# Performance work log

Measured on AMD Instinct MI355X. Metric: run time of the kernel, lower is better.

The kernel has to match this reference:

```python
import jax, jax.numpy as jnp
import numpy as np

S, D, H, G, DH = 2048, 4096, 32, 8, 128  # seq, d_in, heads, kv_groups, head_dim
GROUP = H // G


def rotate_half(x):
    x1, x2 = jnp.split(x, 2, axis=-1)
    return jnp.concatenate([-x2, x1], axis=-1)


def setup_inputs() -> dict:
    key = jax.random.key(0)
    ks = jax.random.split(key, 8)
    x = jax.random.normal(ks[0], (1, S, D), dtype=jnp.float32)
    # causal mask: True above the diagonal (positions to mask out)
    mask = jnp.triu(jnp.ones((S, S), dtype=bool), k=1)
    # standard RoPE tables
    inv_freq = 1.0 / (10000.0 ** (np.arange(0, DH, 2, dtype=np.float32) / DH))
    t = np.arange(S, dtype=np.float32)
    freqs = np.outer(t, inv_freq)                      # [S, DH/2]
    emb = np.concatenate([freqs, freqs], axis=-1)      # [S, DH]
    cos = jnp.asarray(np.cos(emb), dtype=jnp.float32)
    sin = jnp.asarray(np.sin(emb), dtype=jnp.float32)
    sc = 0.02
    Wq = jax.random.normal(ks[1], (D, H * DH), dtype=jnp.float32) * sc
    Wk = jax.random.normal(ks[2], (D, G * DH), dtype=jnp.float32) * sc
    Wv = jax.random.normal(ks[3], (D, G * DH), dtype=jnp.float32) * sc
    Wo = jax.random.normal(ks[4], (H * DH, D), dtype=jnp.float32) * sc
    return {"x": x, "mask": mask, "cos": cos, "sin": sin,
            "Wq": Wq, "Wk": Wk, "Wv": Wv, "Wo": Wo}


def reference(x, mask, cos, sin, Wq, Wk, Wv, Wo):
    xs = x[0]                                          # [S, D] (batch must be 1)
    q = (xs @ Wq).reshape(S, H, DH).transpose(1, 0, 2)   # [H, S, DH]
    k = (xs @ Wk).reshape(S, G, DH).transpose(1, 0, 2)   # [G, S, DH]
    v = (xs @ Wv).reshape(S, G, DH).transpose(1, 0, 2)   # [G, S, DH]
    # RoPE
    q = q * cos[None] + rotate_half(q) * sin[None]
    k = k * cos[None] + rotate_half(k) * sin[None]
    # GQA: repeat KV groups to match query heads
    k = jnp.repeat(k, GROUP, axis=0)                   # [H, S, DH]
    v = jnp.repeat(v, GROUP, axis=0)                   # [H, S, DH]
    scores = jnp.einsum('hsd,htd->hst', q, k)          # [H, S, S]
    scores = jnp.where(mask[None], -jnp.inf, scores)
    scores = scores / jnp.sqrt(jnp.float32(DH))
    w = jax.nn.softmax(scores, axis=-1)
    ctx = jnp.einsum('hst,htd->hsd', w, v)             # [H, S, DH]
    ctx = ctx.transpose(1, 0, 2).reshape(S, H * DH)
    out = ctx @ Wo                                     # [S, D]
    return out[None]                                   # [1, S, D]
```

## Files before the change

kernel.cpp:

```cpp
#include <hip/hip_runtime.h>
#include <hip/hip_bf16.h>
#include <cstdint>
#include <cstddef>

#define S 2048
#define D 4096
#define H 32
#define G 8
#define DH 128
#define HD (H*DH)
#define GD (G*DH)

typedef __bf16 bf16;
typedef __bf16 bf16x4 __attribute__((ext_vector_type(4)));
typedef __bf16 bf16x8 __attribute__((ext_vector_type(8)));
typedef float f32x4 __attribute__((ext_vector_type(4)));

__device__ __forceinline__ void gload16(const void* g, void* l) {
    __builtin_amdgcn_global_load_lds(
        (const __attribute__((address_space(1))) void*)g,
        (__attribute__((address_space(3))) void*)l, 16, 0, 0);
}

#define FENCE() asm volatile("" ::: "memory")
#define BARRIER() do { FENCE(); __builtin_amdgcn_s_barrier(); FENCE(); } while (0)
#define VMCNT(n)  asm volatile("s_waitcnt vmcnt(" #n ")" ::: "memory")
#define LGKM0()   do { asm volatile("s_waitcnt lgkmcnt(0)" ::: "memory"); \
                       __builtin_amdgcn_sched_barrier(0); } while (0)

__global__ __launch_bounds__(256) void prep_fused(
    const float* __restrict__ x, bf16* __restrict__ xb,
    const float* __restrict__ Wq, const float* __restrict__ Wk,
    const float* __restrict__ Wv, bf16* __restrict__ Wqkvt)
{
    const int b = blockIdx.x, tid = threadIdx.x;
    if (b < 512) {
        int i = b * 4096 + tid;
        #pragma unroll
        for (int it = 0; it < 16; ++it, i += 256) {
            float4 v = reinterpret_cast<const float4*>(x)[i];
            bf16x4 o = { (bf16)v.x, (bf16)v.y, (bf16)v.z, (bf16)v.w };
            reinterpret_cast<bf16x4*>(xb)[i] = o;
        }
        return;
    }
    const float* in; bf16* out; int Cc, bx, by;
    if (b < 1536)      { int tb = b - 512;  in = Wq; out = Wqkvt;                       Cc = HD; bx = tb & 15; by = tb >> 4; }
    else if (b < 1792) { int tb = b - 1536; in = Wk; out = Wqkvt + (size_t)HD * D;      Cc = GD; bx = tb & 3;  by = tb >> 2; }
    else               { int tb = b - 1792; in = Wv; out = Wqkvt + (size_t)(HD+GD) * D; Cc = GD; bx = tb & 3;  by = tb >> 2; }
    const int r0 = by * 64 + (tid & 7) * 8;
    const int c0 = bx * 256 + (tid >> 3) * 8;
    bf16 m[8][8];
    #pragma unroll
    for (int j = 0; j < 8; ++j) {
        const float* p = in + (size_t)(r0 + j) * Cc + c0;
        float4 a = *reinterpret_cast<const float4*>(p);
        float4 bq = *reinterpret_cast<const float4*>(p + 4);
        m[j][0] = (bf16)a.x;  m[j][1] = (bf16)a.y;  m[j][2] = (bf16)a.z;  m[j][3] = (bf16)a.w;
        m[j][4] = (bf16)bq.x; m[j][5] = (bf16)bq.y; m[j][6] = (bf16)bq.z; m[j][7] = (bf16)bq.w;
    }
    #pragma unroll
    for (int i = 0; i < 8; ++i) {
        bf16x8 ov;
        #pragma unroll
        for (int j = 0; j < 8; ++j) ov[j] = m[j][i];
        *reinterpret_cast<bf16x8*>(out + (size_t)(c0 + i) * D + r0) = ov;
    }
}

__global__ __launch_bounds__(256) void rope_vt_fused(
    bf16* __restrict__ Qb, bf16* __restrict__ Kb,
    const bf16* __restrict__ Vb, bf16* __restrict__ VtG,
    const float* __restrict__ cosT, const float* __restrict__ sinT, float qs)
{
    const int b = blockIdx.x, tid = threadIdx.x;
    if (b < 20480) {
        bf16* Y; int ncols, idx; float scale;
        if (b < 16384) { Y = Qb; ncols = HD; idx = b * 256 + tid;           scale = qs; }
        else           { Y = Kb; ncols = GD; idx = (b - 16384) * 256 + tid; scale = 1.0f; }
        int pairs = ncols >> 1;
        int s = idx / pairs;
        int p = idx - s * pairs;
        int head = p >> 6;
        int d = p & 63;
        size_t base = (size_t)s * ncols + head * DH;
        float c  = cosT[s * DH + d];
        float sn = sinT[s * DH + d];
        float a = (float)Y[base + d];
        float bb = (float)Y[base + d + 64];
        Y[base + d]      = (bf16)((a * c - bb * sn) * scale);
        Y[base + d + 64] = (bf16)((bb * c + a * sn) * scale);
        return;
    }
    const int tb = b - 20480;
    const int r0 = (tb >> 2) * 64 + (tid & 7) * 8;
    const int c0 = (tb & 3) * 256 + (tid >> 3) * 8;
    bf16 m[8][8];
    #pragma unroll
    for (int j = 0; j < 8; ++j) {
        bf16x8 v = *reinterpret_cast<const bf16x8*>(Vb + (size_t)(r0 + j) * GD + c0);
        #pragma unroll
        for (int i = 0; i < 8; ++i) m[j][i] = v[i];
    }
    #pragma unroll
    for (int i = 0; i < 8; ++i) {
        bf16x8 ov;
        #pragma unroll
        for (int j = 0; j < 8; ++j) ov[j] = m[j][i];
        *reinterpret_cast<bf16x8*>(VtG + (size_t)(c0 + i) * S + r0) = ov;
    }
}

__global__ __launch_bounds__(256) void cast_f32_bf16(const float* __restrict__ in,
                                                     bf16* __restrict__ out, int n4)
{
    int i = blockIdx.x * 256 + threadIdx.x;
    if (i < n4) {
        float4 v = reinterpret_cast<const float4*>(in)[i];
        bf16x4 o = { (bf16)v.x, (bf16)v.y, (bf16)v.z, (bf16)v.w };
        reinterpret_cast<bf16x4*>(out)[i] = o;
    }
}

template<bool IN_F32>
__global__ __launch_bounds__(256) void transpose_to_bf16(
    const void* __restrict__ in, bf16* __restrict__ out, int R, int C)
{
    const int r0 = blockIdx.y * 64 + (threadIdx.x & 7) * 8;
    const int c0 = blockIdx.x * 256 + (threadIdx.x >> 3) * 8;
    bf16 m[8][8];
    #pragma unroll
    for (int j = 0; j < 8; ++j) {
        if constexpr (IN_F32) {
            const float* p = (const float*)in + (size_t)(r0 + j) * C + c0;
            float4 a = *reinterpret_cast<const float4*>(p);
            float4 b = *reinterpret_cast<const float4*>(p + 4);
            m[j][0] = (bf16)a.x; m[j][1] = (bf16)a.y; m[j][2] = (bf16)a.z; m[j][3] = (bf16)a.w;
            m[j][4] = (bf16)b.x; m[j][5] = (bf16)b.y; m[j][6] = (bf16)b.z; m[j][7] = (bf16)b.w;
        } else {
            const bf16* p = (const bf16*)in + (size_t)(r0 + j) * C + c0;
            bf16x8 v = *reinterpret_cast<const bf16x8*>(p);
            #pragma unroll
            for (int i = 0; i < 8; ++i) m[j][i] = v[i];
        }
    }
    #pragma unroll
    for (int i = 0; i < 8; ++i) {
        bf16x8 ov;
        #pragma unroll
        for (int j = 0; j < 8; ++j) ov[j] = m[j][i];
        *reinterpret_cast<bf16x8*>(out + (size_t)(c0 + i) * R + r0) = ov;
    }
}

__global__ __launch_bounds__(256) void rope_inplace(bf16* __restrict__ Y,
                                                    const float* __restrict__ cosT,
                                                    const float* __restrict__ sinT,
                                                    int ncols, int total, float scale)
{
    int idx = blockIdx.x * 256 + threadIdx.x;
    if (idx >= total) return;
    int pairs = ncols >> 1;
    int s = idx / pairs;
    int p = idx - s * pairs;
    int head = p >> 6;
    int d = p & 63;
    size_t base = (size_t)s * ncols + head * DH;
    float c  = cosT[s * DH + d];
    float sn = sinT[s * DH + d];
    float a = (float)Y[base + d];
    float b = (float)Y[base + d + 64];
    Y[base + d]      = (bf16)((a * c - b * sn) * scale);
    Y[base + d + 64] = (bf16)((b * c + a * sn) * scale);
}

__global__ __launch_bounds__(512) void gemm8p(
    const bf16* __restrict__ A, const bf16* __restrict__ Bt,
    bf16* __restrict__ Qout, bf16* __restrict__ Kout, bf16* __restrict__ Vout,
    const float* __restrict__ WoIn, bf16* __restrict__ WotOut,
    int N, int K, int ngemm)
{
    extern __shared__ char smem[];
    const int tid = threadIdx.x;

    if ((int)blockIdx.x >= ngemm) {
        const int tb = blockIdx.x - ngemm;
        const int r0 = tb * 64 + (tid & 7) * 8;
        #pragma unroll 1
        for (int pass = 0; pass < 8; ++pass) {
            const int c0 = pass * 512 + (tid >> 3) * 8;
            bf16 m[8][8];
            #pragma unroll
            for (int j = 0; j < 8; ++j) {
                const float* p = WoIn + (size_t)(r0 + j) * D + c0;
                float4 a = *reinterpret_cast<const float4*>(p);
                float4 b = *reinterpret_cast<const float4*>(p + 4);
                m[j][0] = (bf16)a.x; m[j][1] = (bf16)a.y; m[j][2] = (bf16)a.z; m[j][3] = (bf16)a.w;
                m[j][4] = (bf16)b.x; m[j][5] = (bf16)b.y; m[j][6] = (bf16)b.z; m[j][7] = (bf16)b.w;
            }
            #pragma unroll
            for (int i = 0; i < 8; ++i) {
                bf16x8 ov;
                #pragma unroll
                for (int j = 0; j < 8; ++j) ov[j] = m[j][i];
                *reinterpret_cast<bf16x8*>(WotOut + (size_t)(c0 + i) * HD + r0) = ov;
            }
        }
        return;
    }

    const int lane = tid & 63, wave = tid >> 6;
    const int wr = wave >> 2, wc = wave & 3;
    const int l15 = lane & 15, lhi = lane >> 4;
    const int r8 = lane >> 3, c8 = lane & 7;
    const int csw = ((c8 ^ r8) << 3);

    const int x = blockIdx.x & 7, i = blockIdx.x >> 3;
    const int brow = (x >> 2) * 4 + (i & 3);
    const int bcol = (x & 3) * 6 + (i >> 2);
    const int bm = brow * 256, bn = bcol * 256;
    const int NT = K >> 6;

    auto stageA = [&](int buf, int h, int t) {
        #pragma unroll
        for (int L = 0; L < 2; ++L) {
            int row0 = L * 128 + h * 64 + wave * 8;
            gload16(A + (size_t)(bm + row0 + r8) * K + (t << 6) + csw,
                    smem + buf * 65536 + row0 * 128);
        }
    };
    auto stageB = [&](int buf, int h, int t) {
        #pragma unroll
        for (int L = 0; L < 2; ++L) {
            int row0 = h * 128 + L * 64 + wave * 8;
            gload16(Bt + (size_t)(bn + row0 + r8) * K + (t << 6) + csw,
                    smem + buf * 65536 + 32768 + row0 * 128);
        }
    };
    auto rdA = [&](const char* Ab, int mh, int ks, bf16x8* af) {
        #pragma unroll
        for (int m = 0; m < 4; ++m) {
            int row = wr * 128 + mh * 64 + m * 16 + l15;
            int ch = (ks * 4 + lhi) ^ (l15 & 7);
            af[m] = *reinterpret_cast<const bf16x8*>(Ab + row * 128 + ch * 16);
        }
    };
    auto rdB = [&](const char* Bb, int ks, bf16x8* bfv) {
        #pragma unroll
        for (int n = 0; n < 4; ++n) {
            int row = wc * 64 + n * 16 + l15;
            int ch = (ks * 4 + lhi) ^ (l15 & 7);
            bfv[n] = *reinterpret_cast<const bf16x8*>(Bb + row * 128 + ch * 16);
        }
    };

    f32x4 acc[8][4] = {};

    auto mm = [&](int mh, const bf16x8* af, const bf16x8* bfv) {
        LGKM0();
        __builtin_amdgcn_s_setprio(1);
        #pragma unroll
        for (int m = 0; m < 4; ++m)
            #pragma unroll
            for (int n = 0; n < 4; ++n)
                acc[mh * 4 + m][n] = __builtin_amdgcn_mfma_f32_16x16x32_bf16(
                    af[m], bfv[n], acc[mh * 4 + m][n], 0, 0, 0);
        __builtin_amdgcn_s_setprio(0);
    };

    stageA(0, 0, 0); stageA(0, 1, 0); stageB(0, 0, 0); stageB(0, 1, 0);
    stageA(1, 0, 1);
    VMCNT(2);
    BARRIER();

    const char* A0 = smem;
    const char* B0 = smem + 32768;
    const char* A1 = smem + 65536;
    const char* B1 = smem + 65536 + 32768;

    for (int j = 0; j < (NT >> 1); ++j) {
        const int tb = 2 * j + 1;
        const int t2 = (2 * j + 2 < NT) ? 2 * j + 2 : NT - 1;
        const int t3 = (2 * j + 3 < NT) ? 2 * j + 3 : NT - 1;
        bf16x8 af[4], bk0[4], bk1[4];

        rdB(B0, 0, bk0); rdA(A0, 0, 0, af);
        stageA(1, 1, tb);
        mm(0, af, bk0);
        BARRIER();

        rdB(B0, 1, bk1); rdA(A0, 0, 1, af);
        stageB(1, 0, tb);
        mm(0, af, bk1);
        BARRIER();

        rdA(A0, 1, 0, af);
        stageB(1, 1, tb);
        mm(1, af, bk0);
        BARRIER();

        rdA(A0, 1, 1, af);
        stageA(0, 0, t2);
        mm(1, af, bk1);
        VMCNT(2);
        BARRIER();

        rdB(B1, 0, bk0); rdA(A1, 0, 0, af);
        stageA(0, 1, t2);
        mm(0, af, bk0);
        BARRIER();

        rdB(B1, 1, bk1); rdA(A1, 0, 1, af);
        stageB(0, 0, t2);
        mm(0, af, bk1);
        BARRIER();

        rdA(A1, 1, 0, af);
        stageB(0, 1, t2);
        mm(1, af, bk0);
        BARRIER();

        rdA(A1, 1, 1, af);
        stageA(1, 0, t3);
        mm(1, af, bk1);
        VMCNT(2);
        BARRIER();
    }

    #pragma unroll
    for (int m = 0; m < 8; ++m) {
        int r0 = bm + wr * 128 + m * 16 + lhi * 4;
        #pragma unroll
        for (int n = 0; n < 4; ++n) {
            int c = bn + wc * 64 + n * 16 + l15;
            #pragma unroll
            for (int j = 0; j < 4; ++j) {
                bf16 v = (bf16)acc[m][n][j];
                if (bn < HD)
                    Qout[(size_t)(r0 + j) * HD + c] = v;
                else if (bn < HD + GD)
                    Kout[(size_t)(r0 + j) * GD + (c - HD)] = v;
                else
                    Vout[(size_t)(r0 + j) * GD + (c - HD - GD)] = v;
            }
        }
    }
}

__global__ __launch_bounds__(512, 2) void gemm3b(
    const bf16* __restrict__ A, const bf16* __restrict__ Bt,
    float* __restrict__ C, int N, int K)
{
    extern __shared__ char smem[];
    const int tid = threadIdx.x, lane = tid & 63, wave = tid >> 6;
    const int wr = wave >> 1, wc = wave & 1;
    const int l15 = lane & 15, lhi = lane >> 4;
    const int r8 = lane >> 3, c8 = lane & 7;
    const int csw = ((c8 ^ r8) << 3);

    const int x = blockIdx.x & 7, i = blockIdx.x >> 3;
    const int brow = (x >> 2) * 4 + (i & 3);
    const int bcol = (x & 3) * 8 + (i >> 2);
    const int bm = brow * 256, bn = bcol * 128;
    const int NT = K >> 6;

    auto stageA = [&](int buf, int L, int t) {
        int row0 = L * 64 + wave * 8;
        gload16(A + (size_t)(bm + row0 + r8) * K + (t << 6) + csw,
                smem + buf * 49152 + row0 * 128);
    };
    auto stageB = [&](int buf, int L, int t) {
        int row0 = L * 64 + wave * 8;
        gload16(Bt + (size_t)(bn + row0 + r8) * K + (t << 6) + csw,
                smem + buf * 49152 + 32768 + row0 * 128);
    };
    auto rdA = [&](const char* Ab, int ks, bf16x8* af) {
        #pragma unroll
        for (int m = 0; m < 4; ++m) {
            int row = wr * 64 + m * 16 + l15;
            int ch = (ks * 4 + lhi) ^ (l15 & 7);
            af[m] = *reinterpret_cast<const bf16x8*>(Ab + row * 128 + ch * 16);
        }
    };
    auto rdB = [&](const char* Bb, int ks, bf16x8* bfv) {
        #pragma unroll
        for (int n = 0; n < 4; ++n) {
            int row = wc * 64 + n * 16 + l15;
            int ch = (ks * 4 + lhi) ^ (l15 & 7);
            bfv[n] = *reinterpret_cast<const bf16x8*>(Bb + row * 128 + ch * 16);
        }
    };

    f32x4 acc[4][4] = {};

    #pragma unroll
    for (int L = 0; L < 4; ++L) stageA(0, L, 0);
    stageB(0, 0, 0); stageB(0, 1, 0);
    #pragma unroll
    for (int L = 0; L < 4; ++L) stageA(1, L, (1 < NT) ? 1 : 0);
    stageB(1, 0, (1 < NT) ? 1 : 0); stageB(1, 1, (1 < NT) ? 1 : 0);
    VMCNT(6);
    BARRIER();

    for (int t = 0; t < NT; ++t) {
        const char* Ab = smem + (t % 3) * 49152;
        const char* Bb = Ab + 32768;
        const int b2 = (t + 2) % 3;
        const int st = (t + 2 < NT) ? t + 2 : NT - 1;
        bf16x8 af[4], bk[4];

        rdB(Bb, 0, bk); rdA(Ab, 0, af);
        stageA(b2, 0, st); stageA(b2, 1, st);
        LGKM0();
        __builtin_amdgcn_s_setprio(1);
        #pragma unroll
        for (int m = 0; m < 4; ++m)
            #pragma unroll
            for (int n = 0; n < 4; ++n)
                acc[m][n] = __builtin_amdgcn_mfma_f32_16x16x32_bf16(af[m], bk[n], acc[m][n], 0, 0, 0);
        __builtin_amdgcn_s_setprio(0);

        rdB(Bb, 1, bk); rdA(Ab, 1, af);
        stageA(b2, 2, st); stageA(b2, 3, st);
        stageB(b2, 0, st); stageB(b2, 1, st);
        LGKM0();
        __builtin_amdgcn_s_setprio(1);
        #pragma unroll
        for (int m = 0; m < 4; ++m)
            #pragma unroll
            for (int n = 0; n < 4; ++n)
                acc[m][n] = __builtin_amdgcn_mfma_f32_16x16x32_bf16(af[m], bk[n], acc[m][n], 0, 0, 0);
        __builtin_amdgcn_s_setprio(0);

        VMCNT(6);
        BARRIER();
    }

    #pragma unroll
    for (int m = 0; m < 4; ++m) {
        int r0 = bm + wr * 64 + m * 16 + lhi * 4;
        #pragma unroll
        for (int n = 0; n < 4; ++n) {
            int c = bn + wc * 64 + n * 16 + l15;
            #pragma unroll
            for (int j = 0; j < 4; ++j)
                C[(size_t)(r0 + j) * N + c] = acc[m][n][j];
        }
    }
}

#define BM 128
#define BN 128
#define BK 32
#define LDSK 40

template<bool OUT_BF16>
__global__ __launch_bounds__(256) void gemm_aBf16(
    const bf16* __restrict__ A,
    const float* __restrict__ B0, const float* __restrict__ B1,
    void* __restrict__ C0, void* __restrict__ C1,
    int M, int N, int K)
{
    __shared__ alignas(16) bf16 Al[BM][LDSK];
    __shared__ alignas(16) bf16 Bt[BN][LDSK];

    const float* __restrict__ B = blockIdx.z ? B1 : B0;
    void* __restrict__ C = blockIdx.z ? C1 : C0;

    const int tid  = threadIdx.x;
    const int lane = tid & 63;
    const int wave = tid >> 6;
    const int wm = (wave >> 1) * 64;
    const int wn = (wave & 1) * 64;
    const int bm = blockIdx.y * BM;
    const int bn = blockIdx.x * BN;
    const int l15 = lane & 15;
    const int lhi = lane >> 4;

    f32x4 acc[4][4] = {};

    for (int k0 = 0; k0 < K; k0 += BK) {
        #pragma unroll
        for (int it = 0; it < 2; ++it) {
            int idx = it * 256 + tid;
            int row = idx >> 2;
            int ko  = idx & 3;
            bf16x8 v = *reinterpret_cast<const bf16x8*>(
                A + (size_t)(bm + row) * K + k0 + ko * 8);
            *reinterpret_cast<bf16x8*>(&Al[row][ko * 8]) = v;
        }
        {
            int n = tid & 127;
            int kbase = (tid >> 7) * 8;
            const float* bp = B + (size_t)k0 * N + bn + n;
            #pragma unroll
            for (int half = 0; half < 2; ++half) {
                bf16x8 v;
                #pragma unroll
                for (int j = 0; j < 8; ++j)
                    v[j] = (bf16)bp[(size_t)(half * 16 + kbase + j) * N];
                *reinterpret_cast<bf16x8*>(&Bt[n][half * 16 + kbase]) = v;
            }
        }
        __syncthreads();

        bf16x8 af[4], bfv[4];
        #pragma unroll
        for (int m = 0; m < 4; ++m)
            af[m] = *reinterpret_cast<const bf16x8*>(&Al[wm + m * 16 + l15][lhi * 8]);
        #pragma unroll
        for (int n = 0; n < 4; ++n)
            bfv[n] = *reinterpret_cast<const bf16x8*>(&Bt[wn + n * 16 + l15][lhi * 8]);
        #pragma unroll
        for (int m = 0; m < 4; ++m)
            #pragma unroll
            for (int n = 0; n < 4; ++n)
                acc[m][n] = __builtin_amdgcn_mfma_f32_16x16x32_bf16(
                    af[m], bfv[n], acc[m][n], 0, 0, 0);
        __syncthreads();
    }

    #pragma unroll
    for (int m = 0; m < 4; ++m) {
        int r0 = bm + wm + m * 16 + lhi * 4;
        #pragma unroll
        for (int n = 0; n < 4; ++n) {
            int c = bn + wn + n * 16 + l15;
            #pragma unroll
            for (int j = 0; j < 4; ++j) {
                if constexpr (OUT_BF16)
                    reinterpret_cast<bf16*>(C)[(size_t)(r0 + j) * N + c] = (bf16)acc[m][n][j];
                else
                    reinterpret_cast<float*>(C)[(size_t)(r0 + j) * N + c] = acc[m][n][j];
            }
        }
    }
}

#define QBLK 128
#define KVBLK 64
#define NQT (S/QBLK)

template<bool MASK>
__device__ __forceinline__ void attn_tile(
    int t0, int q0w, int l15, int lhi,
    const bf16x8* qf, const char* Kl, const char* Vl, char* Plw,
    f32x4* o, float& m_i, float& l_i)
{
    f32x4 sc[4] = {};
    __builtin_amdgcn_s_setprio(1);
    #pragma unroll
    for (int n = 0; n < 4; ++n) {
        int row = n * 16 + l15;
        #pragma unroll
        for (int kk = 0; kk < 4; ++kk) {
            bf16x8 kf = *reinterpret_cast<const bf16x8*>(
                Kl + row * 256 + ((((kk * 4 + lhi)) ^ (l15 & 7)) << 4));
            sc[n] = __builtin_amdgcn_mfma_f32_16x16x32_bf16(kf, qf[kk], sc[n], 0, 0, 0);
        }
    }
    __builtin_amdgcn_s_setprio(0);

    const int qr = q0w + l15;
    float vals[16];
    #pragma unroll
    for (int n = 0; n < 4; ++n)
        #pragma unroll
        for (int j = 0; j < 4; ++j) {
            float v = sc[n][j];
            if constexpr (MASK) {
                int t = t0 + n * 16 + lhi * 4 + j;
                if (t > qr) v = -1e30f;
            }
            vals[n * 4 + j] = v;
        }

    float m8[8], m4[4];
    #pragma unroll
    for (int k = 0; k < 8; ++k) m8[k] = fmaxf(vals[k], vals[k + 8]);
    #pragma unroll
    for (int k = 0; k < 4; ++k) m4[k] = fmaxf(m8[k], m8[k + 4]);
    float mx = fmaxf(fmaxf(m4[0], m4[1]), fmaxf(m4[2], m4[3]));
    mx = fmaxf(mx, __shfl_xor(mx, 16));
    mx = fmaxf(mx, __shfl_xor(mx, 32));

    const float mnew = (mx <= m_i + 8.0f) ? m_i : mx;
    const float cr = exp2f(m_i - mnew);

    float p[16];
    #pragma unroll
    for (int k = 0; k < 16; ++k) p[k] = exp2f(vals[k] - mnew);
    float s8[8], s4[4];
    #pragma unroll
    for (int k = 0; k < 8; ++k) s8[k] = p[k] + p[k + 8];
    #pragma unroll
    for (int k = 0; k < 4; ++k) s4[k] = s8[k] + s8[k + 4];
    float rsum = (s4[0] + s4[1]) + (s4[2] + s4[3]);
    rsum += __shfl_xor(rsum, 16);
    rsum += __shfl_xor(rsum, 32);
    l_i = l_i * cr + rsum;
    m_i = mnew;

    #pragma unroll
    for (int n = 0; n < 4; ++n) {
        bf16x4 w = { (bf16)p[n*4+0], (bf16)p[n*4+1], (bf16)p[n*4+2], (bf16)p[n*4+3] };
        int off = (l15 << 7) + (((n << 5) + (lhi << 3)) ^ ((l15 & 7) << 4));
        *reinterpret_cast<bf16x4*>(Plw + off) = w;
    }

    float corr[4];
    #pragma unroll
    for (int j = 0; j < 4; ++j) corr[j] = __shfl(cr, lhi * 4 + j, 16);
    if ((corr[0] != 1.f) | (corr[1] != 1.f) | (corr[2] != 1.f) | (corr[3] != 1.f)) {
        #pragma unroll
        for (int n = 0; n < 8; ++n)
            #pragma unroll
            for (int j = 0; j < 4; ++j)
                o[n][j] *= corr[j];
    }

    __builtin_amdgcn_s_setprio(1);
    #pragma unroll
    for (int kk = 0; kk < 2; ++kk) {
        bf16x8 pf = *reinterpret_cast<const bf16x8*>(
            Plw + (l15 << 7) + ((((kk * 4 + lhi)) ^ (l15 & 7)) << 4));
        #pragma unroll
        for (int n = 0; n < 8; ++n) {
            int d = n * 16 + l15;
            bf16x8 vf = *reinterpret_cast<const bf16x8*>(
                Vl + (d << 7) + ((((kk * 4 + lhi)) ^ (d & 7)) << 4));
            o[n] = __builtin_amdgcn_mfma_f32_16x16x32_bf16(pf, vf, o[n], 0, 0, 0);
        }
    }
    __builtin_amdgcn_s_setprio(0);
}

__global__ __launch_bounds__(512) void flash_fwd6(
    const bf16* __restrict__ Q, const bf16* __restrict__ Kr,
    const bf16* __restrict__ VtG, bf16* __restrict__ ctx)
{
    extern __shared__ char fsm[];

    const int tid  = threadIdx.x;
    const int lane = tid & 63;
    const int wave = tid >> 6;
    const int l15 = lane & 15;
    const int lhi = lane >> 4;
    const int bid = blockIdx.x;
    const int qt = (NQT - 1) - (bid >> 5);
    const int h  = ((bid & 7) << 2) | ((bid >> 3) & 3);
    const int g  = h >> 2;
    const int q0 = qt * QBLK;
    const int q0w = q0 + wave * 16;
    char* Plw = fsm + 65536 + wave * 2048;

    bf16x8 qf[4];
    {
        const bf16* qp = Q + (size_t)(q0w + l15) * HD + h * DH + lhi * 8;
        #pragma unroll
        for (int kk = 0; kk < 4; ++kk)
            qf[kk] = *reinterpret_cast<const bf16x8*>(qp + kk * 32);
    }

    f32x4 o[8] = {};
    float m_i = -1e30f;
    float l_i = 0.f;

    auto stage = [&](int t0, int buf) {
        char* Kl = fsm + buf * 32768;
        char* Vl = Kl + 16384;
        #pragma unroll
        for (int t = 0; t < 2; ++t) {
            int ch = t * 512 + tid;
            {
                int row = ch >> 4, ci = ch & 15;
                gload16(Kr + (size_t)(t0 + row) * GD + g * DH + ((ci ^ (row & 7)) << 3),
                        Kl + ch * 16);
            }
            {
                int d = ch >> 3, ci = ch & 7;
                gload16(VtG + (size_t)(g * DH + d) * S + t0 + ((ci ^ (d & 7)) << 3),
                        Vl + ch * 16);
            }
        }
    };

    const int nt = 2 * qt + 2;
    stage(0, 0);
    VMCNT(0);
    BARRIER();

    for (int it = 0; it < nt; ++it) {
        if (it + 1 < nt) stage((it + 1) * KVBLK, (it + 1) & 1);
        const char* Kl = fsm + (it & 1) * 32768;
        const char* Vl = Kl + 16384;
        if (it >= nt - 2)
            attn_tile<true>(it * KVBLK, q0w, l15, lhi, qf, Kl, Vl, Plw, o, m_i, l_i);
        else
            attn_tile<false>(it * KVBLK, q0w, l15, lhi, qf, Kl, Vl, Plw, o, m_i, l_i);
        VMCNT(0);
        BARRIER();
    }

    float lf[4];
    #pragma unroll
    for (int j = 0; j < 4; ++j) lf[j] = __shfl(l_i, lhi * 4 + j, 16);

    #pragma unroll
    for (int n = 0; n < 8; ++n) {
        int c = h * DH + n * 16 + l15;
        #pragma unroll
        for (int j = 0; j < 4; ++j) {
            int r = q0w + lhi * 4 + j;
            ctx[(size_t)r * HD + c] = (bf16)(o[n][j] / lf[j]);
        }
    }
}

extern "C" void kernel_launch(void* const* d_in, const int* in_sizes, int n_in,
                              void* d_out, int out_size, void* d_ws, size_t ws_size,
                              hipStream_t stream)
{
    const float* x    = (const float*)d_in[0];
    const float* cosT = (const float*)d_in[2];
    const float* sinT = (const float*)d_in[3];
    const float* Wq   = (const float*)d_in[4];
    const float* Wk   = (const float*)d_in[5];
    const float* Wv   = (const float*)d_in[6];
    const float* Wo   = (const float*)d_in[7];
    float* out = (float*)d_out;

    const size_t MB = (size_t)1 << 20;
    char* ws = (char*)d_ws;
    bf16* xb  = (bf16*)ws;
    bf16* ctx = (bf16*)(ws + 16 * MB);
    bf16* Qb  = (bf16*)d_out;
    bf16* Kb  = Qb + (size_t)S * HD;
    bf16* Vb  = Kb + (size_t)S * GD;
    bf16* VtG = Vb + (size_t)S * GD;

    const bool fast = ws_size >= 112 * MB;
    const float qscale = 0.08838834764831845f * 1.4426950408889634f;

    hipFuncSetAttribute(reinterpret_cast<const void*>(&flash_fwd6),
                        hipFuncAttributeMaxDynamicSharedMemorySize, 81920);

    if (fast) {
        bf16* Wqkvt = (bf16*)(ws + 32 * MB);
        bf16* Wot   = (bf16*)(ws + 80 * MB);

        hipFuncSetAttribute(reinterpret_cast<const void*>(&gemm8p),
                            hipFuncAttributeMaxDynamicSharedMemorySize, 131072);
        hipFuncSetAttribute(reinterpret_cast<const void*>(&gemm3b),
                            hipFuncAttributeMaxDynamicSharedMemorySize, 147456);

        prep_fused<<<2048, 256, 0, stream>>>(x, xb, Wq, Wk, Wv, Wqkvt);

        gemm8p<<<256, 512, 131072, stream>>>(
            xb, Wqkvt, Qb, Kb, Vb, Wo, Wot, HD + 2 * GD, D, 192);

        rope_vt_fused<<<20608, 256, 0, stream>>>(Qb, Kb, Vb, VtG, cosT, sinT, qscale);

        flash_fwd6<<<NQT * H, 512, 81920, stream>>>(Qb, Kb, VtG, ctx);

        gemm3b<<<256, 512, 147456, stream>>>(ctx, Wot, out, D, HD);
    } else {
        cast_f32_bf16<<<(S * D / 4 + 255) / 256, 256, 0, stream>>>(x, xb, S * D / 4);

        gemm_aBf16<true><<<dim3(HD / BN, S / BM, 1), 256, 0, stream>>>(
            xb, Wq, Wq, (void*)Qb, (void*)Qb, S, HD, D);
        gemm_aBf16<true><<<dim3(GD / BN, S / BM, 2), 256, 0, stream>>>(
            xb, Wk, Wv, (void*)Kb, (void*)Vb, S, GD, D);

        rope_inplace<<<(S * HD / 2 + 255) / 256, 256, 0, stream>>>(Qb, cosT, sinT, HD, S * HD / 2, qscale);
        rope_inplace<<<(S * GD / 2 + 255) / 256, 256, 0, stream>>>(Kb, cosT, sinT, GD, S * GD / 2, 1.0f);

        transpose_to_bf16<false><<<dim3(GD / 256, S / 64), 256, 0, stream>>>(Vb, VtG, S, GD);

        flash_fwd6<<<NQT * H, 512, 81920, stream>>>(Qb, Kb, VtG, ctx);

        gemm_aBf16<false><<<dim3(D / BN, S / BM, 1), 256, 0, stream>>>(
            ctx, Wo, Wo, (void*)out, (void*)out, S, D, HD);
    }

    (void)in_sizes; (void)n_in; (void)out_size; (void)ws_size;
}
```

Before: 319.0 us.

## Retile QKV GEMM to 256x192 tiles over all blocks and move Wo prep

```diff
diff --git a/kernel.cpp b/kernel.cpp
--- a/kernel.cpp
+++ b/kernel.cpp
@@ -31,7 +31,8 @@
 __global__ __launch_bounds__(256) void prep_fused(
     const float* __restrict__ x, bf16* __restrict__ xb,
     const float* __restrict__ Wq, const float* __restrict__ Wk,
-    const float* __restrict__ Wv, bf16* __restrict__ Wqkvt)
+    const float* __restrict__ Wv, const float* __restrict__ Wo,
+    bf16* __restrict__ Wqkvt, bf16* __restrict__ Wot)
 {
     const int b = blockIdx.x, tid = threadIdx.x;
     if (b < 512) {
@@ -47,7 +48,8 @@
     const float* in; bf16* out; int Cc, bx, by;
     if (b < 1536)      { int tb = b - 512;  in = Wq; out = Wqkvt;                       Cc = HD; bx = tb & 15; by = tb >> 4; }
     else if (b < 1792) { int tb = b - 1536; in = Wk; out = Wqkvt + (size_t)HD * D;      Cc = GD; bx = tb & 3;  by = tb >> 2; }
-    else               { int tb = b - 1792; in = Wv; out = Wqkvt + (size_t)(HD+GD) * D; Cc = GD; bx = tb & 3;  by = tb >> 2; }
+    else if (b < 2048) { int tb = b - 1792; in = Wv; out = Wqkvt + (size_t)(HD+GD) * D; Cc = GD; bx = tb & 3;  by = tb >> 2; }
+    else               { int tb = b - 2048; in = Wo; out = Wot;                         Cc = D;  bx = tb & 15; by = tb >> 4; }
     const int r0 = by * 64 + (tid & 7) * 8;
     const int c0 = bx * 256 + (tid >> 3) * 8;
     bf16 m[8][8];
@@ -174,174 +176,110 @@
     Y[base + d + 64] = (bf16)((b * c + a * sn) * scale);
 }
 
-__global__ __launch_bounds__(512) void gemm8p(
+__global__ __launch_bounds__(512) void gemm192q(
     const bf16* __restrict__ A, const bf16* __restrict__ Bt,
-    bf16* __restrict__ Qout, bf16* __restrict__ Kout, bf16* __restrict__ Vout,
-    const float* __restrict__ WoIn, bf16* __restrict__ WotOut,
-    int N, int K, int ngemm)
+    bf16* __restrict__ Qout, bf16* __restrict__ Kout, bf16* __restrict__ Vout, int K)
 {
     extern __shared__ char smem[];
-    const int tid = threadIdx.x;
-
-    if ((int)blockIdx.x >= ngemm) {
-        const int tb = blockIdx.x - ngemm;
-        const int r0 = tb * 64 + (tid & 7) * 8;
-        #pragma unroll 1
-        for (int pass = 0; pass < 8; ++pass) {
-            const int c0 = pass * 512 + (tid >> 3) * 8;
-            bf16 m[8][8];
-            #pragma unroll
-            for (int j = 0; j < 8; ++j) {
-                const float* p = WoIn + (size_t)(r0 + j) * D + c0;
-                float4 a = *reinterpret_cast<const float4*>(p);
-                float4 b = *reinterpret_cast<const float4*>(p + 4);
-                m[j][0] = (bf16)a.x; m[j][1] = (bf16)a.y; m[j][2] = (bf16)a.z; m[j][3] = (bf16)a.w;
-                m[j][4] = (bf16)b.x; m[j][5] = (bf16)b.y; m[j][6] = (bf16)b.z; m[j][7] = (bf16)b.w;
-            }
-            #pragma unroll
-            for (int i = 0; i < 8; ++i) {
-                bf16x8 ov;
-                #pragma unroll
-                for (int j = 0; j < 8; ++j) ov[j] = m[j][i];
-                *reinterpret_cast<bf16x8*>(WotOut + (size_t)(c0 + i) * HD + r0) = ov;
-            }
-        }
-        return;
-    }
-
-    const int lane = tid & 63, wave = tid >> 6;
+    const int tid = threadIdx.x, lane = tid & 63, wave = tid >> 6;
     const int wr = wave >> 2, wc = wave & 3;
     const int l15 = lane & 15, lhi = lane >> 4;
     const int r8 = lane >> 3, c8 = lane & 7;
     const int csw = ((c8 ^ r8) << 3);
 
-    const int x = blockIdx.x & 7, i = blockIdx.x >> 3;
-    const int brow = (x >> 2) * 4 + (i & 3);
-    const int bcol = (x & 3) * 6 + (i >> 2);
-    const int bm = brow * 256, bn = bcol * 256;
+    const int x = blockIdx.x & 7, bi = blockIdx.x >> 3;
+    const int brow = (x >> 2) * 4 + (bi & 3);
+    const int bcol = (x & 3) * 8 + (bi >> 2);
+    const int bm = brow * 256, bn = bcol * 192;
     const int NT = K >> 6;
 
-    auto stageA = [&](int buf, int h, int t) {
-        #pragma unroll
-        for (int L = 0; L < 2; ++L) {
-            int row0 = L * 128 + h * 64 + wave * 8;
-            gload16(A + (size_t)(bm + row0 + r8) * K + (t << 6) + csw,
-                    smem + buf * 65536 + row0 * 128);
-        }
-    };
-    auto stageB = [&](int buf, int h, int t) {
-        #pragma unroll
-        for (int L = 0; L < 2; ++L) {
-            int row0 = h * 128 + L * 64 + wave * 8;
-            gload16(Bt + (size_t)(bn + row0 + r8) * K + (t << 6) + csw,
-                    smem + buf * 65536 + 32768 + row0 * 128);
-        }
-    };
-    auto rdA = [&](const char* Ab, int mh, int ks, bf16x8* af) {
+    auto stA = [&](int buf, int h, int L, int t) {
+        int row0 = L * 128 + h * 64 + wave * 8;
+        gload16(A + (size_t)(bm + row0 + r8) * K + (t << 6) + csw,
+                smem + buf * 57344 + row0 * 128);
+    };
+    auto stB = [&](int buf, int u, int t) {
+        int row0 = u * 64 + wave * 8;
+        gload16(Bt + (size_t)(bn + row0 + r8) * K + (t << 6) + csw,
+                smem + buf * 57344 + 32768 + row0 * 128);
+    };
+    auto rdA = [&](const char* Cb, int mh, int ks, bf16x8* af) {
         #pragma unroll
         for (int m = 0; m < 4; ++m) {
             int row = wr * 128 + mh * 64 + m * 16 + l15;
             int ch = (ks * 4 + lhi) ^ (l15 & 7);
-            af[m] = *reinterpret_cast<const bf16x8*>(Ab + row * 128 + ch * 16);
-        }
-    };
-    auto rdB = [&](const char* Bb, int ks, bf16x8* bfv) {
-        #pragma unroll
-        for (int n = 0; n < 4; ++n) {
-            int row = wc * 64 + n * 16 + l15;
+            af[m] = *reinterpret_cast<const bf16x8*>(Cb + row * 128 + ch * 16);
+        }
+    };
+    auto rdB = [&](const char* Cb, int ks, bf16x8* bfv) {
+        #pragma unroll
+        for (int n = 0; n < 3; ++n) {
+            int row = wc * 48 + n * 16 + l15;
             int ch = (ks * 4 + lhi) ^ (l15 & 7);
-            bfv[n] = *reinterpret_cast<const bf16x8*>(Bb + row * 128 + ch * 16);
-        }
-    };
-
-    f32x4 acc[8][4] = {};
-
+            bfv[n] = *reinterpret_cast<const bf16x8*>(Cb + 32768 + row * 128 + ch * 16);
+        }
+    };
+
+    f32x4 acc[8][3] = {};
     auto mm = [&](int mh, const bf16x8* af, const bf16x8* bfv) {
         LGKM0();
         __builtin_amdgcn_s_setprio(1);
         #pragma unroll
         for (int m = 0; m < 4; ++m)
             #pragma unroll
-            for (int n = 0; n < 4; ++n)
+            for (int n = 0; n < 3; ++n)
                 acc[mh * 4 + m][n] = __builtin_amdgcn_mfma_f32_16x16x32_bf16(
                     af[m], bfv[n], acc[mh * 4 + m][n], 0, 0, 0);
         __builtin_amdgcn_s_setprio(0);
     };
 
-    stageA(0, 0, 0); stageA(0, 1, 0); stageB(0, 0, 0); stageB(0, 1, 0);
-    stageA(1, 0, 1);
+    stB(0, 0, 0); stB(0, 1, 0); stB(0, 2, 0);
+    stA(0, 0, 0, 0); stA(0, 0, 1, 0);
+    stA(0, 1, 0, 0); stA(0, 1, 1, 0);
     VMCNT(2);
     BARRIER();
 
-    const char* A0 = smem;
-    const char* B0 = smem + 32768;
-    const char* A1 = smem + 65536;
-    const char* B1 = smem + 65536 + 32768;
-
-    for (int j = 0; j < (NT >> 1); ++j) {
-        const int tb = 2 * j + 1;
-        const int t2 = (2 * j + 2 < NT) ? 2 * j + 2 : NT - 1;
-        const int t3 = (2 * j + 3 < NT) ? 2 * j + 3 : NT - 1;
-        bf16x8 af[4], bk0[4], bk1[4];
-
-        rdB(B0, 0, bk0); rdA(A0, 0, 0, af);
-        stageA(1, 1, tb);
+    for (int t = 0; t < NT; ++t) {
+        const char* cur = smem + (t & 1) * 57344;
+        const int nb = (t + 1) & 1;
+        const int tn = (t + 1 < NT) ? t + 1 : t;
+        bf16x8 af[4], bk0[3], bk1[3];
+
+        rdA(cur, 0, 0, af); rdB(cur, 0, bk0);
+        stB(nb, 0, tn); stB(nb, 1, tn);
         mm(0, af, bk0);
         BARRIER();
 
-        rdB(B0, 1, bk1); rdA(A0, 0, 1, af);
-        stageB(1, 0, tb);
+        rdA(cur, 0, 1, af); rdB(cur, 1, bk1);
+        stB(nb, 2, tn); stA(nb, 0, 0, tn);
         mm(0, af, bk1);
+        VMCNT(4);
         BARRIER();
 
-        rdA(A0, 1, 0, af);
-        stageB(1, 1, tb);
+        rdA(cur, 1, 0, af);
+        stA(nb, 0, 1, tn); stA(nb, 1, 0, tn);
         mm(1, af, bk0);
         BARRIER();
 
-        rdA(A0, 1, 1, af);
-        stageA(0, 0, t2);
+        rdA(cur, 1, 1, af);
+        stA(nb, 1, 1, tn);
         mm(1, af, bk1);
         VMCNT(2);
         BARRIER();
-
-        rdB(B1, 0, bk0); rdA(A1, 0, 0, af);
-        stageA(0, 1, t2);
-        mm(0, af, bk0);
-        BARRIER();
-
-        rdB(B1, 1, bk1); rdA(A1, 0, 1, af);
-        stageB(0, 0, t2);
-        mm(0, af, bk1);
-        BARRIER();
-
-        rdA(A1, 1, 0, af);
-        stageB(0, 1, t2);
-        mm(1, af, bk0);
-        BARRIER();
-
-        rdA(A1, 1, 1, af);
-        stageA(1, 0, t3);
-        mm(1, af, bk1);
-        VMCNT(2);
-        BARRIER();
-    }
-
-    #pragma unroll
-    for (int m = 0; m < 8; ++m) {
-        int r0 = bm + wr * 128 + m * 16 + lhi * 4;
-        #pragma unroll
-        for (int n = 0; n < 4; ++n) {
-            int c = bn + wc * 64 + n * 16 + l15;
+    }
+
+    #pragma unroll
+    for (int mm_i = 0; mm_i < 8; ++mm_i) {
+        int r0 = bm + wr * 128 + (mm_i >> 2) * 64 + (mm_i & 3) * 16 + lhi * 4;
+        #pragma unroll
+        for (int n = 0; n < 3; ++n) {
+            int c = bn + wc * 48 + n * 16 + l15;
             #pragma unroll
             for (int j = 0; j < 4; ++j) {
-                bf16 v = (bf16)acc[m][n][j];
-                if (bn < HD)
-                    Qout[(size_t)(r0 + j) * HD + c] = v;
-                else if (bn < HD + GD)
-                    Kout[(size_t)(r0 + j) * GD + (c - HD)] = v;
-                else
-                    Vout[(size_t)(r0 + j) * GD + (c - HD - GD)] = v;
+                bf16 v = (bf16)acc[mm_i][n][j];
+                if (c < HD)            Qout[(size_t)(r0 + j) * HD + c] = v;
+                else if (c < HD + GD)  Kout[(size_t)(r0 + j) * GD + (c - HD)] = v;
+                else                   Vout[(size_t)(r0 + j) * GD + (c - HD - GD)] = v;
             }
         }
     }
@@ -749,15 +687,14 @@
         bf16* Wqkvt = (bf16*)(ws + 32 * MB);
         bf16* Wot   = (bf16*)(ws + 80 * MB);
 
-        hipFuncSetAttribute(reinterpret_cast<const void*>(&gemm8p),
-                            hipFuncAttributeMaxDynamicSharedMemorySize, 131072);
+        hipFuncSetAttribute(reinterpret_cast<const void*>(&gemm192q),
+                            hipFuncAttributeMaxDynamicSharedMemorySize, 114688);
         hipFuncSetAttribute(reinterpret_cast<const void*>(&gemm3b),
                             hipFuncAttributeMaxDynamicSharedMemorySize, 147456);
 
-        prep_fused<<<2048, 256, 0, stream>>>(x, xb, Wq, Wk, Wv, Wqkvt);
-
-        gemm8p<<<256, 512, 131072, stream>>>(
-            xb, Wqkvt, Qb, Kb, Vb, Wo, Wot, HD + 2 * GD, D, 192);
+        prep_fused<<<3072, 256, 0, stream>>>(x, xb, Wq, Wk, Wv, Wo, Wqkvt, Wot);
+
+        gemm192q<<<256, 512, 114688, stream>>>(xb, Wqkvt, Qb, Kb, Vb, D);
 
         rope_vt_fused<<<20608, 256, 0, stream>>>(Qb, Kb, Vb, VtG, cosT, sinT, qscale);
 
```

Result: no change. 320.3 us (+0.4%).
